# Kernel optimization log

Measured on AMD Instinct MI355X. Metric: run time of the kernel, lower is better.

## Reference

```python
import jax, jax.numpy as jnp
import numpy as np

EPS = 1e-6
SCALE_END = 1.0


def _rms_norm(x, w):
    # x: [B, L, H, D], w: [D]
    var = jnp.mean(jnp.square(x), axis=-1, keepdims=True)
    return x * jax.lax.rsqrt(var + EPS) * w


def _apply_rope(x, freqs):
    # x: [B, L, H, D]; freqs: [L, D//2] rotation angles.
    # Interleaved pair rotation: (x0, x1) -> (x0*cos - x1*sin, x0*sin + x1*cos)
    B, L, H, D = x.shape
    xr = x.reshape(B, L, H, D // 2, 2)
    x0, x1 = xr[..., 0], xr[..., 1]
    cos = jnp.cos(freqs)[None, :, None, :]  # [1, L, 1, D//2]
    sin = jnp.sin(freqs)[None, :, None, :]
    o0 = x0 * cos - x1 * sin
    o1 = x0 * sin + x1 * cos
    return jnp.stack([o0, o1], axis=-1).reshape(B, L, H, D)


def setup_inputs() -> dict:
    key = jax.random.key(0)
    ks = jax.random.split(key, 6)
    B, Lq, Lk, H, D = 1, 4096, 1024, 24, 128
    hidden = H * D
    query = jax.random.normal(ks[0], (B, Lq, H, D), dtype=jnp.float32)
    ref_latent = jax.random.normal(ks[1], (B, Lk, hidden), dtype=jnp.float32)
    ref_freqs = jax.random.uniform(ks[2], (Lk, D // 2), dtype=jnp.float32)
    Wk = jax.random.normal(ks[3], (hidden, hidden), dtype=jnp.float32) * (hidden ** -0.5)
    Wv = jax.random.normal(ks[4], (hidden, hidden), dtype=jnp.float32) * (hidden ** -0.5)
    rms_w = jnp.ones((D,), dtype=jnp.float32)
    return {"query": query, "ref_latent": ref_latent, "ref_freqs": ref_freqs,
            "Wk": Wk, "Wv": Wv, "rms_w": rms_w}


def reference(query, ref_latent, ref_freqs, Wk, Wv, rms_w):
    B, Lq, H, D = query.shape
    # K/V projections (nn.Linear: y = x @ W.T)
    ref_k = jnp.einsum('ble,he->blh', ref_latent, Wk).reshape(B, -1, H, D)
    ref_v = jnp.einsum('ble,he->blh', ref_latent, Wv).reshape(B, -1, H, D)
    # RMSNorm on K heads, then rotary embedding on K
    ref_k = _rms_norm(ref_k, rms_w)
    ref_k = _apply_rope(ref_k, ref_freqs)
    # Non-causal attention, softmax_scale = head_dim ** -0.5 (flash_attn layout B L H D)
    scale = D ** -0.5
    scores = jnp.einsum('bqhd,bkhd->bhqk', query, ref_k) * scale
    probs = jax.nn.softmax(scores, axis=-1)
    attn = jnp.einsum('bhqk,bkhd->bqhd', probs, ref_v)
    attn = attn.reshape(B, Lq, H * D)
    return SCALE_END * attn
```

## Files before the change

### kernel.cpp

```cpp
#include <hip/hip_runtime.h>
#include <hip/hip_bf16.h>

typedef __attribute__((ext_vector_type(8))) short short8;
typedef float floatx4 __attribute__((ext_vector_type(4)));
typedef float floatx16 __attribute__((ext_vector_type(16)));

#define LQ 4096
#define LK 1024
#define NH 24
#define HD 128
#define HID 3072

__device__ __forceinline__ unsigned short f2bf(float f) {
    __hip_bfloat16 h = __float2bfloat16(f);
    union { __hip_bfloat16 b; unsigned short u; } c; c.b = h;
    return c.u;
}

__device__ __forceinline__ unsigned cvtpk(float a, float b) {
    unsigned r;
    asm("v_cvt_pk_bf16_f32 %0, %1, %2" : "=v"(r) : "v"(a), "v"(b));
    return r;
}

__device__ __forceinline__ float fexp2(float x) {
    float r;
    asm("v_exp_f32 %0, %1" : "=v"(r) : "v"(x));
    return r;
}

__device__ __forceinline__ void gload16(const void* g, void* l) {
    __builtin_amdgcn_global_load_lds(
        (const __attribute__((address_space(1))) void*)g,
        (__attribute__((address_space(3))) void*)l,
        16, 0, 0);
}

__global__ void f32_to_bf16(const float* __restrict__ in, unsigned short* __restrict__ out, int n4) {
    int i = blockIdx.x * blockDim.x + threadIdx.x;
    int stride = gridDim.x * blockDim.x;
    for (; i < n4; i += stride) {
        float4 v = ((const float4*)in)[i];
        ushort4 o;
        o.x = f2bf(v.x); o.y = f2bf(v.y); o.z = f2bf(v.z); o.w = f2bf(v.w);
        ((ushort4*)out)[i] = o;
    }
}

__global__ __launch_bounds__(256) void gemm_proj(const unsigned short* __restrict__ A,
                                                 const unsigned short* __restrict__ Bw,
                                                 float* __restrict__ C,
                                                 int M, int N, int K) {
    __shared__ __align__(16) unsigned short As[2][64 * 64];
    __shared__ __align__(16) unsigned short Bs[2][128 * 64];
    const int tid = threadIdx.x;
    const int lane = tid & 63;
    const int wave = tid >> 6;
    const int wm = wave >> 1, wn = wave & 1;
    const int flat = blockIdx.x + gridDim.x * blockIdx.y;
    const int wid = (flat & 7) * 48 + (flat >> 3);
    const int bm0 = (wid & 15) * 64;
    const int bn0 = (wid >> 4) * 128;
    const int kbeg = blockIdx.z * (K >> 1);
    const int kend = kbeg + (K >> 1);
    float* Cz = C + (size_t)blockIdx.z * M * N;
    const int lr = lane & 15;
    const int lg = lane >> 4;

    floatx4 acc[2][4];
    for (int i = 0; i < 2; ++i)
        for (int j = 0; j < 4; ++j)
            acc[i][j] = (floatx4){0.f, 0.f, 0.f, 0.f};

    auto stage = [&](int b, int k0) {
        for (int p = 0; p < 2; ++p) {
            int slot = p * 256 + tid;
            int r = slot >> 3, cb = slot & 7;
            int g = cb ^ (r & 7);
            gload16(&A[(bm0 + r) * K + k0 + g * 8], &As[b][(p * 256 + wave * 64) * 8]);
        }
        for (int p = 0; p < 4; ++p) {
            int slot = p * 256 + tid;
            int r = slot >> 3, cb = slot & 7;
            int g = cb ^ (r & 7);
            gload16(&Bw[(bn0 + r) * K + k0 + g * 8], &Bs[b][(p * 256 + wave * 64) * 8]);
        }
    };

    auto compute = [&](int b) {
        for (int ks = 0; ks < 2; ++ks) {
            short8 af[2], bfr[4];
            for (int mt = 0; mt < 2; ++mt) {
                int m = wm * 32 + mt * 16 + lr;
                int sc = (ks * 4 + lg) ^ (m & 7);
                af[mt] = *(const short8*)(&As[b][m * 64 + sc * 8]);
            }
            for (int nt = 0; nt < 4; ++nt) {
                int n = wn * 64 + nt * 16 + lr;
                int sc = (ks * 4 + lg) ^ (n & 7);
                bfr[nt] = *(const short8*)(&Bs[b][n * 64 + sc * 8]);
            }
            __builtin_amdgcn_s_setprio(1);
            for (int mt = 0; mt < 2; ++mt)
                for (int nt = 0; nt < 4; ++nt)
                    acc[mt][nt] = __builtin_amdgcn_mfma_f32_16x16x32_bf16(af[mt], bfr[nt], acc[mt][nt], 0, 0, 0);
            __builtin_amdgcn_s_setprio(0);
        }
    };

    stage(0, kbeg);
    __syncthreads();
    int buf = 0;
    for (int k0 = kbeg; k0 < kend - 64; k0 += 64) {
        stage(buf ^ 1, k0 + 64);
        compute(buf);
        __syncthreads();
        buf ^= 1;
    }
    compute(buf);

    for (int mt = 0; mt < 2; ++mt)
        for (int nt = 0; nt < 4; ++nt)
            for (int rg = 0; rg < 4; ++rg) {
                int m = bm0 + wm * 32 + mt * 16 + lg * 4 + rg;
                int n = bn0 + wn * 64 + nt * 16 + lr;
                Cz[m * N + n] = acc[mt][nt][rg];
            }
}

__global__ __launch_bounds__(256) void rmsnorm_rope(const float* __restrict__ r0,
                                                    const float* __restrict__ r1,
                                                    const float* __restrict__ freqs,
                                                    const float* __restrict__ w,
                                                    unsigned short* __restrict__ Kbf) {
    int row = blockIdx.x * 2 + (threadIdx.x >> 7);
    int l = row / NH, h = row % NH;
    int d = threadIdx.x & 127;
    int idx = l * HID + h * HD + d;
    float x = r0[idx] + r1[idx];
    float ss = x * x;
    for (int off = 32; off; off >>= 1) ss += __shfl_xor(ss, off);
    __shared__ float red[4];
    int wv = threadIdx.x >> 6;
    if ((threadIdx.x & 63) == 0) red[wv] = ss;
    __syncthreads();
    int base = (threadIdx.x >> 7) * 2;
    float tot = red[base] + red[base + 1];
    float rsn = rsqrtf(tot * (1.0f / 128.0f) + 1e-6f);
    float xn = x * rsn * w[d];
    float f = freqs[l * (HD / 2) + (d >> 1)];
    float s = __sinf(f), c = __cosf(f);
    float partner = __shfl_xor(xn, 1);
    float o = (d & 1) ? (partner * s + xn * c) : (xn * c - partner * s);
    Kbf[idx] = f2bf(o);
}

__global__ __launch_bounds__(256) void transpose_v(const float* __restrict__ r0,
                                                   const float* __restrict__ r1,
                                                   unsigned short* __restrict__ Vfrag) {
    __shared__ float tile[32][65];
    const int bx = blockIdx.x;
    const int by = blockIdx.y;
    const int hd0 = bx * 64, l0 = by * 32;
    const int tx = threadIdx.x & 63;
    const int tg8 = threadIdx.x >> 6;
    for (int i = 0; i < 8; ++i) {
        int r = tg8 * 8 + i;
        int idx = (l0 + r) * HID + hd0 + tx;
        tile[r][tx] = r0[idx] + r1[idx];
    }
    __syncthreads();
    const int tg = threadIdx.x >> 6;
    const int c = tg >> 1, hi = tg & 1;
    const int hdl = threadIdx.x & 63;
    const int kloc = c * 16 + hi * 8;
    short8 v;
    for (int j = 0; j < 8; ++j)
        v[j] = (short)f2bf(tile[kloc + j][hdl]);
    const int hd = hd0 + hdl;
    const int h = hd >> 7;
    const int ntd = (hd & 127) >> 5;
    const int l31 = hd & 31;
    size_t pos = ((((size_t)(h * 32 + by) * 4 + ntd) * 2 + c) * 2 + hi) * 32 + l31;
    *(short8*)(&Vfrag[pos * 8]) = v;
}

__global__ __launch_bounds__(256, 3) void attn(const float* __restrict__ Q,
                                               const unsigned short* __restrict__ Kbf,
                                               const unsigned short* __restrict__ Vfrag,
                                               float* __restrict__ O) {
    __shared__ __align__(16) unsigned short KA[2][32 * 128];
    __shared__ __align__(16) unsigned short KB[2][32 * 128];
    __shared__ __align__(16) unsigned short VA[32 * 128];
    __shared__ __align__(16) unsigned short VB[32 * 128];
    const int tid = threadIdx.x;
    const int lane = tid & 63;
    const int wave = tid >> 6;
    const int l31 = lane & 31;
    const int hi = lane >> 5;
    const int flat = blockIdx.x + gridDim.x * blockIdx.y;
    const int wid = (flat & 7) * 96 + (flat >> 3);
    const int h = wid >> 5;
    const int q0 = (wid & 31) * 128 + wave * 32;
    const float qscale = 0.08838834764831843f * 1.44269504088896340736f;
    const float SHIFT = 32.0f;

    short8 qf[8];
#pragma unroll
    for (int m = 0; m < 8; ++m) {
        const float* qp = &Q[(q0 + l31) * HID + h * HD + m * 16 + hi * 8];
        float4 lo = *(const float4*)(qp);
        float4 hif = *(const float4*)(qp + 4);
        short8 v;
        v[0] = (short)f2bf(lo.x * qscale);
        v[1] = (short)f2bf(lo.y * qscale);
        v[2] = (short)f2bf(lo.z * qscale);
        v[3] = (short)f2bf(lo.w * qscale);
        v[4] = (short)f2bf(hif.x * qscale);
        v[5] = (short)f2bf(hif.y * qscale);
        v[6] = (short)f2bf(hif.z * qscale);
        v[7] = (short)f2bf(hif.w * qscale);
        qf[m] = v;
    }

    floatx16 accO[4];
#pragma unroll
    for (int i = 0; i < 4; ++i)
#pragma unroll
        for (int r = 0; r < 16; ++r) accO[i][r] = 0.f;
    float psum = 0.f;

    auto stageK = [&](unsigned short* dst, int kt) {
        for (int i = 0; i < 2; ++i) {
            int slot = i * 256 + tid;
            int r = slot >> 4, bb = slot & 15;
            int g = bb ^ (r & 15);
            gload16(&Kbf[(kt * 32 + r) * HID + h * HD + g * 8],
                    &dst[(i * 256 + wave * 64) * 8]);
        }
    };
    auto stageV = [&](unsigned short* dst, int kt) {
        const unsigned short* src = Vfrag + ((size_t)(h * 32 + kt) << 12);
        for (int i = 0; i < 2; ++i) {
            int slot = i * 256 + tid;
            gload16(&src[slot * 8], &dst[(i * 256 + wave * 64) * 8]);
        }
    };

    auto softmax32 = [&](floatx16 s, short8& pa, short8& pb) {
        float e[16];
#pragma unroll
        for (int r = 0; r < 16; ++r) e[r] = fexp2(s[r]);
        {
            float s01 = e[0] + e[1],   s23 = e[2] + e[3];
            float s45 = e[4] + e[5],   s67 = e[6] + e[7];
            float s89 = e[8] + e[9],   sab = e[10] + e[11];
            float scd = e[12] + e[13], sef = e[14] + e[15];
            float t0 = s01 + s23, t1 = s45 + s67, t2 = s89 + sab, t3 = scd + sef;
            psum += (t0 + t1) + (t2 + t3);
        }
        unsigned d0 = cvtpk(e[0], e[1]),   d1 = cvtpk(e[2], e[3]);
        unsigned d2 = cvtpk(e[4], e[5]),   d3 = cvtpk(e[6], e[7]);
        unsigned d4 = cvtpk(e[8], e[9]),   d5 = cvtpk(e[10], e[11]);
        unsigned d6 = cvtpk(e[12], e[13]), d7 = cvtpk(e[14], e[15]);
        asm volatile("v_permlane32_swap_b32 %0, %1" : "+v"(d0), "+v"(d2));
        asm volatile("v_permlane32_swap_b32 %0, %1" : "+v"(d1), "+v"(d3));
        asm volatile("v_permlane32_swap_b32 %0, %1" : "+v"(d4), "+v"(d6));
        asm volatile("v_permlane32_swap_b32 %0, %1" : "+v"(d5), "+v"(d7));
        union { unsigned u[4]; short8 s; } p0, p1;
        p0.u[0] = d0; p0.u[1] = d1; p0.u[2] = d2; p0.u[3] = d3;
        p1.u[0] = d4; p1.u[1] = d5; p1.u[2] = d6; p1.u[3] = d7;
        pa = p0.s; pb = p1.s;
    };

    stageK(KA[0], 0);
    stageK(KB[0], 16);
    asm volatile("s_waitcnt vmcnt(0)" ::: "memory");
    __builtin_amdgcn_s_barrier();

    for (int t = 0; t < 16; ++t) {
        stageV(VA, t);
        stageV(VB, t + 16);
        if (t < 15) {
            stageK(KA[(t + 1) & 1], t + 1);
            stageK(KB[(t + 1) & 1], t + 17);
        }
        floatx16 sA, sB;
#pragma unroll
        for (int r = 0; r < 16; ++r) { sA[r] = -SHIFT; sB[r] = -SHIFT; }
        __builtin_amdgcn_s_setprio(1);
#pragma unroll
        for (int m = 0; m < 8; ++m) {
            int slot = l31 * 16 + ((m * 2 + hi) ^ (l31 & 15));
            short8 kfa = *(const short8*)(&KA[t & 1][slot * 8]);
            short8 kfb = *(const short8*)(&KB[t & 1][slot * 8]);
            sA = __builtin_amdgcn_mfma_f32_32x32x16_bf16(kfa, qf[m], sA, 0, 0, 0);
            sB = __builtin_amdgcn_mfma_f32_32x32x16_bf16(kfb, qf[m], sB, 0, 0, 0);
        }
        __builtin_amdgcn_s_setprio(0);
        short8 pA0, pA1, pB0, pB1;
        softmax32(sA, pA0, pA1);
        softmax32(sB, pB0, pB1);
        __syncthreads();
        __builtin_amdgcn_s_setprio(1);
#pragma unroll
        for (int ntd = 0; ntd < 4; ++ntd) {
            int s0 = ((ntd * 2 + 0) * 2 + hi) * 32 + l31;
            int s1 = ((ntd * 2 + 1) * 2 + hi) * 32 + l31;
            short8 vA0 = *(const short8*)(&VA[s0 * 8]);
            short8 vA1 = *(const short8*)(&VA[s1 * 8]);
            short8 vB0 = *(const short8*)(&VB[s0 * 8]);
            short8 vB1 = *(const short8*)(&VB[s1 * 8]);
            accO[ntd] = __builtin_amdgcn_mfma_f32_32x32x16_bf16(pA0, vA0, accO[ntd], 0, 0, 0);
            accO[ntd] = __builtin_amdgcn_mfma_f32_32x32x16_bf16(pA1, vA1, accO[ntd], 0, 0, 0);
            accO[ntd] = __builtin_amdgcn_mfma_f32_32x32x16_bf16(pB0, vB0, accO[ntd], 0, 0, 0);
            accO[ntd] = __builtin_amdgcn_mfma_f32_32x32x16_bf16(pB1, vB1, accO[ntd], 0, 0, 0);
        }
        __builtin_amdgcn_s_setprio(0);
        __syncthreads();
    }

    float s = psum + __shfl_xor(psum, 32);
    float rinv = 1.0f / s;
    float ri[16];
#pragma unroll
    for (int r = 0; r < 16; ++r) {
        int row = (r & 3) + 8 * (r >> 2) + 4 * hi;
        ri[r] = __shfl(rinv, row);
    }
#pragma unroll
    for (int ntd = 0; ntd < 4; ++ntd)
#pragma unroll
        for (int r = 0; r < 16; ++r) {
            int row = (r & 3) + 8 * (r >> 2) + 4 * hi;
            O[(q0 + row) * HID + h * HD + ntd * 32 + l31] = accO[ntd][r] * ri[r];
        }
}

extern "C" void kernel_launch(void* const* d_in, const int* in_sizes, int n_in,
                              void* d_out, int out_size, void* d_ws, size_t ws_size,
                              hipStream_t stream) {
    const float* Q      = (const float*)d_in[0];
    const float* latent = (const float*)d_in[1];
    const float* freqs  = (const float*)d_in[2];
    const float* Wk     = (const float*)d_in[3];
    const float* Wv     = (const float*)d_in[4];
    const float* rmsw   = (const float*)d_in[5];
    float* out = (float*)d_out;
    char* ws = (char*)d_ws;

    unsigned short* latent_bf = (unsigned short*)(ws);
    unsigned short* Wbf       = (unsigned short*)(ws + 6291456);
    float*          raw0      = (float*)(ws + 25165824);
    float*          raw1      = (float*)(ws + 37748736);
    unsigned short* Kbf       = (unsigned short*)(ws + 50331648);
    unsigned short* Vfrag     = (unsigned short*)(ws + 56623104);

    f32_to_bf16<<<2048, 256, 0, stream>>>(latent, latent_bf, (LK * HID) / 4);
    f32_to_bf16<<<2048, 256, 0, stream>>>(Wk, Wbf, (HID * HID) / 4);

    gemm_proj<<<dim3(16, 24, 2), 256, 0, stream>>>(latent_bf, Wbf, raw0, LK, HID, HID);
    rmsnorm_rope<<<(LK * NH) / 2, 256, 0, stream>>>(raw0, raw1, freqs, rmsw, Kbf);

    f32_to_bf16<<<2048, 256, 0, stream>>>(Wv, Wbf, (HID * HID) / 4);
    gemm_proj<<<dim3(16, 24, 2), 256, 0, stream>>>(latent_bf, Wbf, raw0, LK, HID, HID);
    transpose_v<<<dim3(HID / 64, LK / 32), 256, 0, stream>>>(raw0, raw1, Vfrag);

    attn<<<dim3(LQ / 128, NH), 256, 0, stream>>>(Q, Kbf, Vfrag, out);
}
```

Baseline: 161.6 us.

## Fuse RMSNorm+RoPE and V transpose into projection GEMM epilogues

The projection GEMM is restructured so that each block owns a 32-row by one-head (128-column) tile over the full K range, which removes the split-K partial outputs. RMSNorm and RoPE are then applied in the epilogue for K, and the bf16 fragment transpose is done through LDS for V. The three fp32-to-bf16 conversion launches are merged into one, and the fp32 intermediate round trips plus two elementwise kernels are dropped. The cost is smaller tiles with less MFMA reuse per block and a full-length K loop in each block.

Result: no change. 163.8 us (+1.3%).

```diff
diff --git a/kernel.cpp b/kernel.cpp
--- a/kernel.cpp
+++ b/kernel.cpp
@@ -36,82 +36,91 @@
         16, 0, 0);
 }
 
-__global__ void f32_to_bf16(const float* __restrict__ in, unsigned short* __restrict__ out, int n4) {
+__global__ void cvt_all(const float* __restrict__ latent, const float* __restrict__ Wk,
+                        const float* __restrict__ Wv, unsigned short* __restrict__ lbf,
+                        unsigned short* __restrict__ wkbf, unsigned short* __restrict__ wvbf) {
+    const int n1 = (LK * HID) / 4;
+    const int n2 = (HID * HID) / 4;
+    const int total = n1 + 2 * n2;
     int i = blockIdx.x * blockDim.x + threadIdx.x;
     int stride = gridDim.x * blockDim.x;
-    for (; i < n4; i += stride) {
-        float4 v = ((const float4*)in)[i];
+    for (; i < total; i += stride) {
+        const float4* src; ushort4* dst; int j;
+        if (i < n1)            { src = (const float4*)latent; dst = (ushort4*)lbf;  j = i; }
+        else if (i < n1 + n2)  { src = (const float4*)Wk;     dst = (ushort4*)wkbf; j = i - n1; }
+        else                   { src = (const float4*)Wv;     dst = (ushort4*)wvbf; j = i - n1 - n2; }
+        float4 v = src[j];
         ushort4 o;
         o.x = f2bf(v.x); o.y = f2bf(v.y); o.z = f2bf(v.z); o.w = f2bf(v.w);
-        ((ushort4*)out)[i] = o;
-    }
-}
-
-__global__ __launch_bounds__(256) void gemm_proj(const unsigned short* __restrict__ A,
-                                                 const unsigned short* __restrict__ Bw,
-                                                 float* __restrict__ C,
-                                                 int M, int N, int K) {
-    __shared__ __align__(16) unsigned short As[2][64 * 64];
+        dst[j] = o;
+    }
+}
+
+__global__ __launch_bounds__(256) void gemm_fused(const unsigned short* __restrict__ A,
+                                                  const unsigned short* __restrict__ Bw,
+                                                  const float* __restrict__ freqs,
+                                                  const float* __restrict__ rmsw,
+                                                  unsigned short* __restrict__ Out,
+                                                  int mode) {
+    __shared__ __align__(16) unsigned short As[2][32 * 64];
     __shared__ __align__(16) unsigned short Bs[2][128 * 64];
+    __shared__ float redK[32][4];
     const int tid = threadIdx.x;
     const int lane = tid & 63;
     const int wave = tid >> 6;
-    const int wm = wave >> 1, wn = wave & 1;
-    const int flat = blockIdx.x + gridDim.x * blockIdx.y;
-    const int wid = (flat & 7) * 48 + (flat >> 3);
-    const int bm0 = (wid & 15) * 64;
-    const int bn0 = (wid >> 4) * 128;
-    const int kbeg = blockIdx.z * (K >> 1);
-    const int kend = kbeg + (K >> 1);
-    float* Cz = C + (size_t)blockIdx.z * M * N;
+    const int flat = blockIdx.x;
+    const int wid = (flat & 7) * 96 + (flat >> 3);
+    const int lt = wid & 31;
+    const int h  = wid >> 5;
+    const int bm0 = lt * 32;
+    const int bn0 = h * 128;
     const int lr = lane & 15;
     const int lg = lane >> 4;
 
-    floatx4 acc[2][4];
+    floatx4 acc[2][2];
     for (int i = 0; i < 2; ++i)
-        for (int j = 0; j < 4; ++j)
+        for (int j = 0; j < 2; ++j)
             acc[i][j] = (floatx4){0.f, 0.f, 0.f, 0.f};
 
     auto stage = [&](int b, int k0) {
-        for (int p = 0; p < 2; ++p) {
-            int slot = p * 256 + tid;
-            int r = slot >> 3, cb = slot & 7;
+        {
+            int r = tid >> 3, cb = tid & 7;
             int g = cb ^ (r & 7);
-            gload16(&A[(bm0 + r) * K + k0 + g * 8], &As[b][(p * 256 + wave * 64) * 8]);
+            gload16(&A[(bm0 + r) * HID + k0 + g * 8], &As[b][(wave * 64) * 8]);
         }
         for (int p = 0; p < 4; ++p) {
             int slot = p * 256 + tid;
             int r = slot >> 3, cb = slot & 7;
             int g = cb ^ (r & 7);
-            gload16(&Bw[(bn0 + r) * K + k0 + g * 8], &Bs[b][(p * 256 + wave * 64) * 8]);
+            gload16(&Bw[(bn0 + r) * HID + k0 + g * 8], &Bs[b][(p * 256 + wave * 64) * 8]);
         }
     };
 
     auto compute = [&](int b) {
         for (int ks = 0; ks < 2; ++ks) {
-            short8 af[2], bfr[4];
+            short8 af[2], bfr[2];
             for (int mt = 0; mt < 2; ++mt) {
-                int m = wm * 32 + mt * 16 + lr;
+                int m = mt * 16 + lr;
                 int sc = (ks * 4 + lg) ^ (m & 7);
                 af[mt] = *(const short8*)(&As[b][m * 64 + sc * 8]);
             }
-            for (int nt = 0; nt < 4; ++nt) {
-                int n = wn * 64 + nt * 16 + lr;
+            for (int nt = 0; nt < 2; ++nt) {
+                int n = wave * 32 + nt * 16 + lr;
                 int sc = (ks * 4 + lg) ^ (n & 7);
                 bfr[nt] = *(const short8*)(&Bs[b][n * 64 + sc * 8]);
             }
             __builtin_amdgcn_s_setprio(1);
             for (int mt = 0; mt < 2; ++mt)
-                for (int nt = 0; nt < 4; ++nt)
+                for (int nt = 0; nt < 2; ++nt)
                     acc[mt][nt] = __builtin_amdgcn_mfma_f32_16x16x32_bf16(af[mt], bfr[nt], acc[mt][nt], 0, 0, 0);
             __builtin_amdgcn_s_setprio(0);
         }
     };
 
-    stage(0, kbeg);
+    stage(0, 0);
     __syncthreads();
     int buf = 0;
-    for (int k0 = kbeg; k0 < kend - 64; k0 += 64) {
+    for (int k0 = 0; k0 < HID - 64; k0 += 64) {
         stage(buf ^ 1, k0 + 64);
         compute(buf);
         __syncthreads();
@@ -119,70 +128,62 @@
     }
     compute(buf);
 
-    for (int mt = 0; mt < 2; ++mt)
-        for (int nt = 0; nt < 4; ++nt)
+    if (mode == 0) {
+        float part[2][4];
+        for (int mt = 0; mt < 2; ++mt)
             for (int rg = 0; rg < 4; ++rg) {
-                int m = bm0 + wm * 32 + mt * 16 + lg * 4 + rg;
-                int n = bn0 + wn * 64 + nt * 16 + lr;
-                Cz[m * N + n] = acc[mt][nt][rg];
+                float v0 = acc[mt][0][rg], v1 = acc[mt][1][rg];
+                float s = v0 * v0 + v1 * v1;
+                s += __shfl_xor(s, 1);
+                s += __shfl_xor(s, 2);
+                s += __shfl_xor(s, 4);
+                s += __shfl_xor(s, 8);
+                part[mt][rg] = s;
             }
-}
-
-__global__ __launch_bounds__(256) void rmsnorm_rope(const float* __restrict__ r0,
-                                                    const float* __restrict__ r1,
-                                                    const float* __restrict__ freqs,
-                                                    const float* __restrict__ w,
-                                                    unsigned short* __restrict__ Kbf) {
-    int row = blockIdx.x * 2 + (threadIdx.x >> 7);
-    int l = row / NH, h = row % NH;
-    int d = threadIdx.x & 127;
-    int idx = l * HID + h * HD + d;
-    float x = r0[idx] + r1[idx];
-    float ss = x * x;
-    for (int off = 32; off; off >>= 1) ss += __shfl_xor(ss, off);
-    __shared__ float red[4];
-    int wv = threadIdx.x >> 6;
-    if ((threadIdx.x & 63) == 0) red[wv] = ss;
-    __syncthreads();
-    int base = (threadIdx.x >> 7) * 2;
-    float tot = red[base] + red[base + 1];
-    float rsn = rsqrtf(tot * (1.0f / 128.0f) + 1e-6f);
-    float xn = x * rsn * w[d];
-    float f = freqs[l * (HD / 2) + (d >> 1)];
-    float s = __sinf(f), c = __cosf(f);
-    float partner = __shfl_xor(xn, 1);
-    float o = (d & 1) ? (partner * s + xn * c) : (xn * c - partner * s);
-    Kbf[idx] = f2bf(o);
-}
-
-__global__ __launch_bounds__(256) void transpose_v(const float* __restrict__ r0,
-                                                   const float* __restrict__ r1,
-                                                   unsigned short* __restrict__ Vfrag) {
-    __shared__ float tile[32][65];
-    const int bx = blockIdx.x;
-    const int by = blockIdx.y;
-    const int hd0 = bx * 64, l0 = by * 32;
-    const int tx = threadIdx.x & 63;
-    const int tg8 = threadIdx.x >> 6;
-    for (int i = 0; i < 8; ++i) {
-        int r = tg8 * 8 + i;
-        int idx = (l0 + r) * HID + hd0 + tx;
-        tile[r][tx] = r0[idx] + r1[idx];
-    }
-    __syncthreads();
-    const int tg = threadIdx.x >> 6;
-    const int c = tg >> 1, hi = tg & 1;
-    const int hdl = threadIdx.x & 63;
-    const int kloc = c * 16 + hi * 8;
-    short8 v;
-    for (int j = 0; j < 8; ++j)
-        v[j] = (short)f2bf(tile[kloc + j][hdl]);
-    const int hd = hd0 + hdl;
-    const int h = hd >> 7;
-    const int ntd = (hd & 127) >> 5;
-    const int l31 = hd & 31;
-    size_t pos = ((((size_t)(h * 32 + by) * 4 + ntd) * 2 + c) * 2 + hi) * 32 + l31;
-    *(short8*)(&Vfrag[pos * 8]) = v;
+        if (lr == 0)
+            for (int mt = 0; mt < 2; ++mt)
+                for (int rg = 0; rg < 4; ++rg)
+                    redK[mt * 16 + lg * 4 + rg][wave] = part[mt][rg];
+        __syncthreads();
+        for (int mt = 0; mt < 2; ++mt)
+            for (int rg = 0; rg < 4; ++rg) {
+                int row = mt * 16 + lg * 4 + rg;
+                float tot = (redK[row][0] + redK[row][1]) + (redK[row][2] + redK[row][3]);
+                float rsn = rsqrtf(tot * (1.0f / 128.0f) + 1e-6f);
+                int l = bm0 + row;
+                for (int nt = 0; nt < 2; ++nt) {
+                    int d = wave * 32 + nt * 16 + lr;
+                    float xn = acc[mt][nt][rg] * rsn * rmsw[d];
+                    float f = freqs[l * (HD / 2) + (d >> 1)];
+                    float sn = __sinf(f), cs = __cosf(f);
+                    float partner = __shfl_xor(xn, 1);
+                    float o = (d & 1) ? (partner * sn + xn * cs) : (xn * cs - partner * sn);
+                    Out[l * HID + bn0 + d] = f2bf(o);
+                }
+            }
+    } else {
+        __syncthreads();
+        float* Ct = (float*)&Bs[0][0];
+        for (int mt = 0; mt < 2; ++mt)
+            for (int nt = 0; nt < 2; ++nt)
+                for (int rg = 0; rg < 4; ++rg)
+                    Ct[(mt * 16 + lg * 4 + rg) * 132 + wave * 32 + nt * 16 + lr] = acc[mt][nt][rg];
+        __syncthreads();
+        unsigned short* dst = Out + (((size_t)(h * 32 + lt)) << 12);
+        for (int p = 0; p < 2; ++p) {
+            int slot = p * 256 + tid;
+            int l31v = slot & 31;
+            int hi2 = (slot >> 5) & 1;
+            int c2 = (slot >> 6) & 1;
+            int ntd = slot >> 7;
+            int col = ntd * 32 + l31v;
+            int r0 = c2 * 16 + hi2 * 8;
+            short8 v;
+            for (int j = 0; j < 8; ++j)
+                v[j] = (short)f2bf(Ct[(r0 + j) * 132 + col]);
+            *(short8*)(&dst[slot * 8]) = v;
+        }
+    }
 }
 
 __global__ __launch_bounds__(256, 3) void attn(const float* __restrict__ Q,
@@ -350,21 +351,13 @@
     char* ws = (char*)d_ws;
 
     unsigned short* latent_bf = (unsigned short*)(ws);
-    unsigned short* Wbf       = (unsigned short*)(ws + 6291456);
-    float*          raw0      = (float*)(ws + 25165824);
-    float*          raw1      = (float*)(ws + 37748736);
-    unsigned short* Kbf       = (unsigned short*)(ws + 50331648);
-    unsigned short* Vfrag     = (unsigned short*)(ws + 56623104);
-
-    f32_to_bf16<<<2048, 256, 0, stream>>>(latent, latent_bf, (LK * HID) / 4);
-    f32_to_bf16<<<2048, 256, 0, stream>>>(Wk, Wbf, (HID * HID) / 4);
-
-    gemm_proj<<<dim3(16, 24, 2), 256, 0, stream>>>(latent_bf, Wbf, raw0, LK, HID, HID);
-    rmsnorm_rope<<<(LK * NH) / 2, 256, 0, stream>>>(raw0, raw1, freqs, rmsw, Kbf);
-
-    f32_to_bf16<<<2048, 256, 0, stream>>>(Wv, Wbf, (HID * HID) / 4);
-    gemm_proj<<<dim3(16, 24, 2), 256, 0, stream>>>(latent_bf, Wbf, raw0, LK, HID, HID);
-    transpose_v<<<dim3(HID / 64, LK / 32), 256, 0, stream>>>(raw0, raw1, Vfrag);
-
+    unsigned short* Wk_bf     = (unsigned short*)(ws + 6291456);
+    unsigned short* Wv_bf     = (unsigned short*)(ws + 25165824);
+    unsigned short* Kbf       = (unsigned short*)(ws + 44040192);
+    unsigned short* Vfrag     = (unsigned short*)(ws + 50331648);
+
+    cvt_all<<<2048, 256, 0, stream>>>(latent, Wk, Wv, latent_bf, Wk_bf, Wv_bf);
+    gemm_fused<<<768, 256, 0, stream>>>(latent_bf, Wk_bf, freqs, rmsw, Kbf, 0);
+    gemm_fused<<<768, 256, 0, stream>>>(latent_bf, Wv_bf, freqs, rmsw, Vfrag, 1);
     attn<<<dim3(LQ / 128, NH), 256, 0, stream>>>(Q, Kbf, Vfrag, out);
 }
```
